# Kernel optimization log

Measured on AMD Instinct MI355X. Metric: run time of the kernel, lower is better.

## Reference

```python
import jax, jax.numpy as jnp
import numpy as np

B, S, QD, KVD, H = 8, 1024, 1024, 1024, 8
NEG_SLOPE = 0.01


def _lin(t, w, b):
    # torch nn.Linear: y = x @ W^T + b, W is (out, in)
    return t @ w.T + b


def _heads(t, n_head):
    b, s, e = t.shape
    return t.reshape(b, s, n_head, e // n_head).transpose(0, 2, 1, 3)  # (B,H,S,D)


def _merge(t):
    b, h, s, d = t.shape
    return t.transpose(0, 2, 1, 3).reshape(b, s, h * d)


def setup_inputs() -> dict:
    key = jax.random.key(0)
    ks = iter(jax.random.split(key, 64))

    def W(shape):
        return (jax.random.normal(next(ks), shape, jnp.float32) * 0.02)

    inp = {
        'x': jax.random.normal(next(ks), (B, S, QD), jnp.float32),
        'y': jax.random.normal(next(ks), (B, S, KVD), jnp.float32),
        # cross-attention projections
        'ca_q_w': W((QD, QD)), 'ca_q_b': W((QD,)),
        'ca_qv_w': W((QD, QD)), 'ca_qv_b': W((QD,)),
        'ca_k_w': W((QD, KVD)), 'ca_k_b': W((QD,)),
        'ca_kv_w': W((QD, KVD)), 'ca_kv_b': W((QD,)),
        'ca_o_w': W((QD, QD)), 'ca_o_b': W((QD,)),
        # LayerNorm over [seq_len, q_dim]
        'ln_w': jnp.ones((S, QD), jnp.float32),
        'ln_b': jnp.zeros((S, QD), jnp.float32),
        # 3-layer FeedForward
        'ff1_w': W((QD, QD)), 'ff1_b': W((QD,)),
        'ff2_w': W((QD, QD)), 'ff2_b': W((QD,)),
        'ff3_w': W((QD, QD)), 'ff3_b': W((QD,)),
        # self-attention 1
        'sa1_q_w': W((QD, QD)), 'sa1_q_b': W((QD,)),
        'sa1_k_w': W((QD, QD)), 'sa1_k_b': W((QD,)),
        'sa1_v_w': W((QD, QD)), 'sa1_v_b': W((QD,)),
        'sa1_o_w': W((QD, QD)), 'sa1_o_b': W((QD,)),
        # self-attention 2
        'sa2_q_w': W((QD, QD)), 'sa2_q_b': W((QD,)),
        'sa2_k_w': W((QD, QD)), 'sa2_k_b': W((QD,)),
        'sa2_v_w': W((QD, QD)), 'sa2_v_b': W((QD,)),
        'sa2_o_w': W((QD, QD)), 'sa2_o_b': W((QD,)),
    }
    return inp


def _self_attn(t, qw, qb, kw, kb, vw, vb, ow, ob):
    q = _heads(_lin(t, qw, qb), H)
    k = _heads(_lin(t, kw, kb), H)
    v = _heads(_lin(t, vw, vb), H)
    scale = 1.0 / jnp.sqrt(jnp.asarray(q.shape[-1], q.dtype))
    a = jax.nn.softmax(jnp.einsum('bhsd,bhtd->bhst', q, k) * scale, axis=-1)
    return _lin(_merge(jnp.einsum('bhst,bhtd->bhsd', a, v)), ow, ob)


def reference(x, y, ca_q_w, ca_q_b, ca_qv_w, ca_qv_b, ca_k_w, ca_k_b, ca_kv_w, ca_kv_b, ca_o_w, ca_o_b, ln_w, ln_b, ff1_w, ff1_b, ff2_w, ff2_b, ff3_w, ff3_b, sa1_q_w, sa1_q_b, sa1_k_w, sa1_k_b, sa1_v_w, sa1_v_b, sa1_o_w, sa1_o_b, sa2_q_w, sa2_q_b, sa2_k_w, sa2_k_b, sa2_v_w, sa2_v_b, sa2_o_w, sa2_o_b):
    # --- FlowFace cross-attention (no 1/sqrt(d) scaling, +QV term) ---
    q = _heads(_lin(x, ca_q_w, ca_q_b), H)
    qv = _heads(_lin(x, ca_qv_w, ca_qv_b), H)
    k = _heads(_lin(y, ca_k_w, ca_k_b), H)
    kv = _heads(_lin(y, ca_kv_w, ca_kv_b), H)
    attn = jax.nn.softmax(jnp.einsum('bhsd,bhtd->bhst', q, k), axis=-1)
    ca = _lin(_merge(jnp.einsum('bhst,bhtd->bhsd', attn, kv) + qv), ca_o_w, ca_o_b)
    h1 = x + ca
    # --- LayerNorm over last two dims [seq_len, q_dim] ---
    mu = h1.mean(axis=(-2, -1), keepdims=True)
    var = h1.var(axis=(-2, -1), keepdims=True)
    hn = (h1 - mu) / jnp.sqrt(var + 1e-5) * ln_w + ln_b
    # --- 3-layer FeedForward with leaky_relu + residual ---
    lr = lambda t: jax.nn.leaky_relu(t, NEG_SLOPE)
    f = lr(_lin(lr(_lin(lr(_lin(hn, ff1_w, ff1_b)), ff2_w, ff2_b)), ff3_w, ff3_b))
    h2 = hn + f
    # --- two self-attention layers ---
    h3 = _self_attn(h2, sa1_q_w, sa1_q_b, sa1_k_w, sa1_k_b, sa1_v_w, sa1_v_b, sa1_o_w, sa1_o_b)
    out = _self_attn(h3, sa2_q_w, sa2_q_b, sa2_k_w, sa2_k_b, sa2_v_w, sa2_v_b, sa2_o_w, sa2_o_b)
    return out
```

## Files before the change

### kernel.cpp

```cpp
#include <hip/hip_runtime.h>
#include <cstdint>
#include <cstddef>

#define DI __device__ __forceinline__

typedef __bf16 bf16x8 __attribute__((ext_vector_type(8)));
typedef float  f32x4  __attribute__((ext_vector_type(4)));

constexpr int kE = 1024;
constexpr int kM = 8192;
constexpr float kSlope = 0.01f;

DI float bf2f(ushort u) { union { uint32_t i; float f; } v; v.i = ((uint32_t)u) << 16; return v.f; }
DI ushort f2bf(float f) {
    union { float f; uint32_t i; } v; v.f = f;
    return (ushort)((v.i + 0x7FFFu + ((v.i >> 16) & 1u)) >> 16);
}
DI bf16x8 ld8f(const float* p) {
    const float4 f0 = *(const float4*)p;
    const float4 f1 = *(const float4*)(p + 4);
    union { bf16x8 v; ushort u[8]; } o;
    o.u[0] = f2bf(f0.x); o.u[1] = f2bf(f0.y); o.u[2] = f2bf(f0.z); o.u[3] = f2bf(f0.w);
    o.u[4] = f2bf(f1.x); o.u[5] = f2bf(f1.y); o.u[6] = f2bf(f1.z); o.u[7] = f2bf(f1.w);
    return o.v;
}
template<typename T> DI float ldf(const T* p);
template<> DI float ldf<ushort>(const ushort* p) { return bf2f(*p); }
template<> DI float ldf<float>(const float* p) { return *p; }

DI void gload16(const void* g, void* lds) {
    __builtin_amdgcn_global_load_lds((const __attribute__((address_space(1))) void*)g,
                                     (__attribute__((address_space(3))) void*)lds, 16, 0, 0);
}

DI int swz7(int r) { return ((r ^ (r >> 3)) & 7) << 4; }

struct PtrTab { const float* w[16]; const float* b[16]; const float* x; const float* y; };

__global__ __launch_bounds__(256)
void cvt_pack(PtrTab t, ushort* __restrict__ WB, ushort* __restrict__ Xb,
              ushort* __restrict__ Yb, float* __restrict__ BP)
{
    const int blk = blockIdx.x, tid = threadIdx.x;
    if (blk < 16384) {
        const float* src; ushort* dst; size_t idx;
        if (blk < 8192)       { const int w = blk >> 9; idx = (size_t)(blk & 511) * 2048 + tid * 8; src = t.w[w]; dst = WB + (size_t)w * 1048576; }
        else if (blk < 12288) { idx = (size_t)(blk - 8192) * 2048 + tid * 8;  src = t.x; dst = Xb; }
        else                  { idx = (size_t)(blk - 12288) * 2048 + tid * 8; src = t.y; dst = Yb; }
        *(bf16x8*)(dst + idx) = ld8f(src + idx);
    } else {
        const size_t i = (size_t)(blk - 16384) * 2048 + tid * 8;
        const int w = (int)(i >> 10), off = (int)(i & 1023);
        *(float4*)(BP + i)     = *(const float4*)(t.b[w] + off);
        *(float4*)(BP + i + 4) = *(const float4*)(t.b[w] + off + 4);
    }
}

template<int ACT, int RESID, int VT, typename TR, typename TO>
__global__ __launch_bounds__(256)
void gemm_bf16(const ushort* __restrict__ A, const ushort* __restrict__ W,
               const float* __restrict__ bias, const TR* __restrict__ resb,
               TO* __restrict__ out, int N, ushort* __restrict__ vt_out, int vtcol0,
               float oscale)
{
    __shared__ __align__(16) char sm[2][16384];
    constexpr int K = 1024;
    const int tid = threadIdx.x, l = tid & 63, wid = tid >> 6;
    const int wm = wid >> 1, wn = wid & 1;

    const int cpx = gridDim.x >> 3;
    const int sb = (blockIdx.x & 7) * cpx + (blockIdx.x >> 3);
    const int slab = sb >> 9, rr = sb & 511;
    const int bm = rr >> 3, bn = (slab << 3) + (rr & 7);
    const size_t row0 = (size_t)bm << 7, col0 = (size_t)bn << 7;
    const bool isvt = VT && ((int)col0 >= vtcol0);

    const int o0 = (wid * 2) * 1024 + (l << 4), o1 = o0 + 1024;
    const int r0s = o0 >> 6, c0s = ((o0 >> 4) & 3) ^ ((r0s >> 1) & 3);
    const int r1s = o1 >> 6, c1s = ((o1 >> 4) & 3) ^ ((r1s >> 1) & 3);
    const ushort* gA0 = A + (row0 + r0s) * K + c0s * 8;
    const ushort* gA1 = A + (row0 + r1s) * K + c1s * 8;
    const ushort* gW0 = W + (col0 + r0s) * K + c0s * 8;
    const ushort* gW1 = W + (col0 + r1s) * K + c1s * 8;
    const int d0 = (wid * 2) * 1024, d1 = d0 + 1024;

    f32x4 acc[4][4] = {};

    {
        gload16(gA0, sm[0] + d0); gload16(gA1, sm[0] + d1);
        gload16(gW0, sm[0] + 8192 + d0); gload16(gW1, sm[0] + 8192 + d1);
    }
    __syncthreads();

    for (int kt = 0; kt < 32; ++kt) {
        const int cur = kt & 1;
        if (kt + 1 < 32) {
            const int ko = (kt + 1) << 5;
            char* nb = sm[cur ^ 1];
            gload16(gA0 + ko, nb + d0); gload16(gA1 + ko, nb + d1);
            gload16(gW0 + ko, nb + 8192 + d0); gload16(gW1 + ko, nb + 8192 + d1);
        }
        const char* At = sm[cur];
        const char* Wt = sm[cur] + 8192;
        bf16x8 af[4], bfr[4];
        #pragma unroll
        for (int mi = 0; mi < 4; ++mi) {
            const int r = (wm << 6) + (mi << 4) + (l & 15);
            af[mi] = *(const bf16x8*)(At + r * 64 + ((((l >> 4) ^ ((r >> 1) & 3))) << 4));
        }
        #pragma unroll
        for (int ni = 0; ni < 4; ++ni) {
            const int r = (wn << 6) + (ni << 4) + (l & 15);
            bfr[ni] = *(const bf16x8*)(Wt + r * 64 + ((((l >> 4) ^ ((r >> 1) & 3))) << 4));
        }
        if (!isvt) {
            #pragma unroll
            for (int mi = 0; mi < 4; ++mi)
                #pragma unroll
                for (int ni = 0; ni < 4; ++ni)
                    acc[mi][ni] = __builtin_amdgcn_mfma_f32_16x16x32_bf16(af[mi], bfr[ni], acc[mi][ni], 0, 0, 0);
        } else {
            #pragma unroll
            for (int mi = 0; mi < 4; ++mi)
                #pragma unroll
                for (int ni = 0; ni < 4; ++ni)
                    acc[mi][ni] = __builtin_amdgcn_mfma_f32_16x16x32_bf16(bfr[ni], af[mi], acc[mi][ni], 0, 0, 0);
        }
        __syncthreads();
    }

    const int cr = (l >> 4) << 2, cc = l & 15;
    if (!isvt) {
        #pragma unroll
        for (int mi = 0; mi < 4; ++mi) {
            #pragma unroll
            for (int ni = 0; ni < 4; ++ni) {
                const size_t gr = row0 + (wm << 6) + (mi << 4) + cr;
                const size_t gc = col0 + (wn << 6) + (ni << 4) + cc;
                const float bv = bias[gc];
                #pragma unroll
                for (int r = 0; r < 4; ++r) {
                    float v = (acc[mi][ni][r] + bv) * oscale;
                    if (ACT) v = v > 0.f ? v : v * kSlope;
                    const size_t off = (gr + r) * (size_t)N + gc;
                    if (RESID) v += ldf(resb + off);
                    if constexpr (sizeof(TO) == 4) out[off] = v;
                    else                           out[off] = f2bf(v);
                }
            }
        }
    } else if (VT) {
        #pragma unroll
        for (int mi = 0; mi < 4; ++mi) {
            const size_t t_glob = row0 + (wm << 6) + (mi << 4) + cc;
            const size_t bb = t_glob >> 10;
            const int tt = (int)(t_glob & 1023);
            #pragma unroll
            for (int ni = 0; ni < 4; ++ni) {
                const int gcb = (int)col0 + (wn << 6) + (ni << 4) + cr;
                const int dbase = gcb - vtcol0;
                #pragma unroll
                for (int r = 0; r < 4; ++r) {
                    const float v = acc[mi][ni][r] + bias[gcb + r];
                    vt_out[(((bb << 10) + dbase + r) << 10) + tt] = f2bf(v);
                }
            }
        }
    }
}

template<int ADD_QV>
__global__ __launch_bounds__(256)
void attn_fwd(const ushort* __restrict__ Q, const ushort* __restrict__ K,
              const ushort* __restrict__ VT, const ushort* __restrict__ QV,
              ushort* __restrict__ O, int ld)
{
    __shared__ __align__(16) char Kt[64 * 256];
    __shared__ __align__(16) char Vt[128 * 128];
    __shared__ __align__(16) char Pl[4][2048];

    const int tid = threadIdx.x;
    const int l = tid & 63, w = tid >> 6;

    const int cpx = gridDim.x >> 3;
    const int sb = (blockIdx.x & 7) * cpx + (blockIdx.x >> 3);
    const int qt = sb & 15;
    const int bh = sb >> 4;
    const int h = bh & 7, b = bh >> 3;

    const size_t bi = ((size_t)b << 10) * (size_t)ld + ((size_t)h << 7);
    const size_t bo = ((size_t)b << 10) * 1024 + ((size_t)h << 7);
    const size_t vtoff = ((size_t)bh) << 17;
    const size_t qrow0 = (size_t)(qt << 6) + (w << 4);

    bf16x8 qf[4];
    #pragma unroll
    for (int kk = 0; kk < 4; ++kk)
        qf[kk] = *(const bf16x8*)(Q + bi + (qrow0 + (l & 15)) * ld + (kk << 5) + ((l >> 4) << 3));

    f32x4 oacc[8] = {};
    f32x4 lacc = {};
    float mrow[4] = {-1e30f, -1e30f, -1e30f, -1e30f};

    bf16x8 vones;
    #pragma unroll
    for (int j = 0; j < 8; ++j) vones[j] = (__bf16)1.0f;

    const int sr = tid >> 4, sc = tid & 15;

    int vofs[4];
    #pragma unroll
    for (int it = 0; it < 4; ++it) {
        const int d = it * 32 + (tid >> 3);
        const int s = tid & 7;
        const int c = s ^ ((d ^ (d >> 3)) & 7);
        vofs[it] = d * 1024 + c * 8;
    }
    const int vdst = tid * 16;

    for (int kt0 = 0; kt0 < 16; ++kt0) {
        __syncthreads();
        #pragma unroll
        for (int it = 0; it < 4; ++it) {
            const int r = sr + (it << 4);
            uint4 kv = *(const uint4*)(K + bi + (size_t)(kt0 * 64 + r) * ld + (sc << 3));
            *(uint4*)(Kt + r * 256 + ((sc << 4) ^ swz7(r))) = kv;
        }
        #pragma unroll
        for (int it = 0; it < 4; ++it) {
            uint4 vv = *(const uint4*)(VT + vtoff + (size_t)(kt0 << 6) + vofs[it]);
            *(uint4*)(Vt + it * 4096 + vdst) = vv;
        }
        __syncthreads();

        f32x4 sacc[4] = {};
        #pragma unroll
        for (int ni = 0; ni < 4; ++ni) {
            const int r = (l & 15) + (ni << 4);
            #pragma unroll
            for (int kk = 0; kk < 4; ++kk) {
                bf16x8 kf = *(const bf16x8*)(Kt + r * 256 + ((((kk << 2) + (l >> 4)) << 4) ^ swz7(r)));
                sacc[ni] = __builtin_amdgcn_mfma_f32_16x16x32_bf16(qf[kk], kf, sacc[ni], 0, 0, 0);
            }
        }

        float m0[4];
        #pragma unroll
        for (int r = 0; r < 4; ++r) {
            float m = fmaxf(fmaxf(sacc[0][r], sacc[1][r]), fmaxf(sacc[2][r], sacc[3][r]));
            #pragma unroll
            for (int msk = 1; msk < 16; msk <<= 1) m = fmaxf(m, __shfl_xor(m, msk, 64));
            m0[r] = m;
        }
        const bool grow = (m0[0] > mrow[0]) || (m0[1] > mrow[1]) ||
                          (m0[2] > mrow[2]) || (m0[3] > mrow[3]);
        if (__any(grow)) {
            float corr[4];
            #pragma unroll
            for (int r = 0; r < 4; ++r) {
                const float mn = fmaxf(mrow[r], m0[r]);
                corr[r] = __expf(mrow[r] - mn);
                mrow[r] = mn;
            }
            #pragma unroll
            for (int nd = 0; nd < 8; ++nd)
                #pragma unroll
                for (int r = 0; r < 4; ++r) oacc[nd][r] *= corr[r];
            #pragma unroll
            for (int r = 0; r < 4; ++r) lacc[r] *= corr[r];
        }

        char* pw = Pl[w];
        #pragma unroll
        for (int r = 0; r < 4; ++r) {
            const int q = ((l >> 4) << 2) + r;
            const int qo = q * 128, qm = swz7(q);
            const float mr = mrow[r];
            #pragma unroll
            for (int ni = 0; ni < 4; ++ni) {
                const float p = __expf(sacc[ni][r] - mr);
                const int t = (l & 15) + (ni << 4);
                *(__bf16*)(pw + qo + ((t * 2) ^ qm)) = (__bf16)p;
            }
        }

        #pragma unroll
        for (int tg = 0; tg < 2; ++tg) {
            const int q = l & 15;
            bf16x8 pf = *(const bf16x8*)(pw + q * 128 + ((((tg << 2) + (l >> 4)) << 4) ^ swz7(q)));
            #pragma unroll
            for (int nd = 0; nd < 8; ++nd) {
                const int d = (nd << 4) + (l & 15);
                const int m = (d ^ (d >> 3)) & 7;
                bf16x8 vf = *(const bf16x8*)(Vt + d * 128 + ((((tg << 2) + (l >> 4)) ^ m) << 4));
                oacc[nd] = __builtin_amdgcn_mfma_f32_16x16x32_bf16(pf, vf, oacc[nd], 0, 0, 0);
            }
            lacc = __builtin_amdgcn_mfma_f32_16x16x32_bf16(pf, vones, lacc, 0, 0, 0);
        }
    }

    const size_t orow = qrow0 + ((l >> 4) << 2);
    #pragma unroll
    for (int r = 0; r < 4; ++r) {
        const float inv = 1.f / lacc[r];
        #pragma unroll
        for (int nd = 0; nd < 8; ++nd) {
            const size_t c = (l & 15) + (nd << 4);
            float v = oacc[nd][r] * inv;
            if (ADD_QV) v += bf2f(QV[bi + (orow + r) * ld + c]);
            O[bo + (orow + r) * 1024 + c] = f2bf(v);
        }
    }
}

__global__ void ln_partial(const ushort* __restrict__ h1, float2* __restrict__ part)
{
    __shared__ float sa[8];
    const size_t off = ((size_t)blockIdx.x) << 15;
    float s = 0.f, s2 = 0.f;
    for (int i = threadIdx.x; i < 4096; i += 256) {
        uint4 u = *(const uint4*)(h1 + off + (size_t)i * 8);
        const ushort* e = (const ushort*)&u;
        #pragma unroll
        for (int j = 0; j < 8; ++j) { const float v = bf2f(e[j]); s += v; s2 += v * v; }
    }
    #pragma unroll
    for (int m = 1; m < 64; m <<= 1) { s += __shfl_xor(s, m, 64); s2 += __shfl_xor(s2, m, 64); }
    const int w = threadIdx.x >> 6;
    if ((threadIdx.x & 63) == 0) { sa[w * 2] = s; sa[w * 2 + 1] = s2; }
    __syncthreads();
    if (threadIdx.x == 0)
        part[blockIdx.x] = make_float2(sa[0] + sa[2] + sa[4] + sa[6], sa[1] + sa[3] + sa[5] + sa[7]);
}

__global__ void ln_finish(const float2* __restrict__ part, float2* __restrict__ stats)
{
    const int b = threadIdx.x;
    if (b < 8) {
        float s = 0.f, s2 = 0.f;
        for (int c = 0; c < 32; ++c) { const float2 v = part[b * 32 + c]; s += v.x; s2 += v.y; }
        const float mu = s * (1.f / 1048576.f);
        const float var = s2 * (1.f / 1048576.f) - mu * mu;
        stats[b] = make_float2(mu, rsqrtf(var + 1e-5f));
    }
}

__global__ void ln_apply(const ushort* __restrict__ h1, const float2* __restrict__ stats,
                         const float* __restrict__ gw, const float* __restrict__ gb,
                         ushort* __restrict__ hn)
{
    const size_t i = ((size_t)blockIdx.x * 256 + threadIdx.x) * 8;
    const int b = (int)(i >> 20);
    const size_t r = i & 1048575;
    const float2 st = stats[b];
    uint4 uv = *(const uint4*)(h1 + i);
    const float4 w0 = *(const float4*)(gw + r);
    const float4 w1 = *(const float4*)(gw + r + 4);
    const float4 b0 = *(const float4*)(gb + r);
    const float4 b1 = *(const float4*)(gb + r + 4);
    const float wv[8] = {w0.x, w0.y, w0.z, w0.w, w1.x, w1.y, w1.z, w1.w};
    const float bv[8] = {b0.x, b0.y, b0.z, b0.w, b1.x, b1.y, b1.z, b1.w};
    const ushort* ev = (const ushort*)&uv;
    ushort o[8];
    #pragma unroll
    for (int j = 0; j < 8; ++j)
        o[j] = f2bf((bf2f(ev[j]) - st.x) * st.y * wv[j] + bv[j]);
    *(uint4*)(hn + i) = *(const uint4*)o;
}

extern "C" void kernel_launch(void* const* d_in, const int* in_sizes, int n_in,
                              void* d_out, int out_size, void* d_ws, size_t ws_size,
                              hipStream_t stream)
{
    (void)in_sizes; (void)n_in; (void)out_size; (void)ws_size;
    auto P = [&](int i) { return (const float*)d_in[i]; };

    const size_t MB = 1u << 20;
    char* ws = (char*)d_ws;
    ushort* WB = (ushort*)ws;
    ushort* B0 = (ushort*)(ws + 32 * MB);
    ushort* B1 = (ushort*)(ws + 48 * MB);
    ushort* B2 = (ushort*)(ws + 64 * MB);
    ushort* B3 = (ushort*)(ws + 80 * MB);
    ushort* B4 = (ushort*)(ws + 96 * MB);
    ushort* B5 = (ushort*)(ws + 112 * MB);
    float*  BP = (float*)(ws + 128 * MB);
    float2* PART = (float2*)(ws + 128 * MB + 65536);
    float2* STATS = PART + 256;

    PtrTab tab;
    const int wsrc[16] = {2,4,6,8,10,14,16,18,20,22,24,26,28,30,32,34};
    for (int i = 0; i < 16; ++i) { tab.w[i] = P(wsrc[i]); tab.b[i] = P(wsrc[i] + 1); }
    tab.x = P(0); tab.y = P(1);

    const dim3 blk(256), gg(512);
    const float SA_SCALE = 0.08838834764831845f;
    auto Wp = [&](int w) { return WB + (size_t)w * 1048576; };
    auto Bp = [&](int w) { return BP + (size_t)w * 1024; };
    const ushort* NUS = nullptr;

    cvt_pack<<<dim3(16392), blk, 0, stream>>>(tab, WB, B4, B5, BP);

    gemm_bf16<0,0,0,ushort,ushort><<<gg, blk, 0, stream>>>(B4, Wp(0), Bp(0), NUS, B0, 1024, nullptr, 0, 1.0f);
    gemm_bf16<0,0,0,ushort,ushort><<<gg, blk, 0, stream>>>(B4, Wp(1), Bp(1), NUS, B1, 1024, nullptr, 0, 1.0f);
    gemm_bf16<0,0,0,ushort,ushort><<<gg, blk, 0, stream>>>(B5, Wp(2), Bp(2), NUS, B2, 1024, nullptr, 0, 1.0f);
    gemm_bf16<0,0,1,ushort,ushort><<<gg, blk, 0, stream>>>(B5, Wp(3), Bp(3), NUS, B3, 1024, B3, 0, 1.0f);
    attn_fwd<1><<<dim3(1024), blk, 0, stream>>>(B0, B2, B3, B1, B4, 1024);
    gemm_bf16<0,1,0,float,ushort><<<gg, blk, 0, stream>>>(B4, Wp(4), Bp(4), P(0), B5, 1024, nullptr, 0, 1.0f);

    ln_partial<<<dim3(256), blk, 0, stream>>>(B5, PART);
    ln_finish<<<dim3(1), dim3(64), 0, stream>>>(PART, STATS);
    ln_apply<<<dim3(4096), blk, 0, stream>>>(B5, STATS, P(12), P(13), B0);

    gemm_bf16<1,0,0,ushort,ushort><<<gg, blk, 0, stream>>>(B0, Wp(5), Bp(5), NUS, B1, 1024, nullptr, 0, 1.0f);
    gemm_bf16<1,0,0,ushort,ushort><<<gg, blk, 0, stream>>>(B1, Wp(6), Bp(6), NUS, B2, 1024, nullptr, 0, 1.0f);
    gemm_bf16<1,1,0,ushort,ushort><<<gg, blk, 0, stream>>>(B2, Wp(7), Bp(7), B0, B3, 1024, nullptr, 0, 1.0f);

    gemm_bf16<0,0,0,ushort,ushort><<<gg, blk, 0, stream>>>(B3, Wp(8),  Bp(8),  NUS, B0, 1024, nullptr, 0, SA_SCALE);
    gemm_bf16<0,0,0,ushort,ushort><<<gg, blk, 0, stream>>>(B3, Wp(9),  Bp(9),  NUS, B1, 1024, nullptr, 0, 1.0f);
    gemm_bf16<0,0,1,ushort,ushort><<<gg, blk, 0, stream>>>(B3, Wp(10), Bp(10), NUS, B2, 1024, B2, 0, 1.0f);
    attn_fwd<0><<<dim3(1024), blk, 0, stream>>>(B0, B1, B2, nullptr, B4, 1024);
    gemm_bf16<0,0,0,ushort,ushort><<<gg, blk, 0, stream>>>(B4, Wp(11), Bp(11), NUS, B5, 1024, nullptr, 0, 1.0f);

    gemm_bf16<0,0,0,ushort,ushort><<<gg, blk, 0, stream>>>(B5, Wp(12), Bp(12), NUS, B0, 1024, nullptr, 0, SA_SCALE);
    gemm_bf16<0,0,0,ushort,ushort><<<gg, blk, 0, stream>>>(B5, Wp(13), Bp(13), NUS, B1, 1024, nullptr, 0, 1.0f);
    gemm_bf16<0,0,1,ushort,ushort><<<gg, blk, 0, stream>>>(B5, Wp(14), Bp(14), NUS, B2, 1024, B2, 0, 1.0f);
    attn_fwd<0><<<dim3(1024), blk, 0, stream>>>(B0, B1, B2, nullptr, B4, 1024);
    gemm_bf16<0,0,0,ushort,float><<<gg, blk, 0, stream>>>(B4, Wp(15), Bp(15), NUS, (float*)d_out, 1024, nullptr, 0, 1.0f);
}
```

Baseline: 763.7 us.

## Double-buffer K/V tiles in attention with async global-to-LDS loads

```diff
diff --git a/kernel.cpp b/kernel.cpp
--- a/kernel.cpp
+++ b/kernel.cpp
@@ -175,8 +175,8 @@
               const ushort* __restrict__ VT, const ushort* __restrict__ QV,
               ushort* __restrict__ O, int ld)
 {
-    __shared__ __align__(16) char Kt[64 * 256];
-    __shared__ __align__(16) char Vt[128 * 128];
+    __shared__ __align__(16) char KB[2][16384];
+    __shared__ __align__(16) char VB[2][16384];
     __shared__ __align__(16) char Pl[4][2048];
 
     const int tid = threadIdx.x;
@@ -206,32 +206,44 @@
     #pragma unroll
     for (int j = 0; j < 8; ++j) vones[j] = (__bf16)1.0f;
 
-    const int sr = tid >> 4, sc = tid & 15;
-
-    int vofs[4];
-    #pragma unroll
-    for (int it = 0; it < 4; ++it) {
-        const int d = it * 32 + (tid >> 3);
-        const int s = tid & 7;
-        const int c = s ^ ((d ^ (d >> 3)) & 7);
-        vofs[it] = d * 1024 + c * 8;
-    }
-    const int vdst = tid * 16;
+    const int kr0 = (w << 4) + 0 + (l >> 4), kr1 = kr0 + 4, kr2 = kr0 + 8, kr3 = kr0 + 12;
+    const int ksl = l & 15;
+    const size_t ks0 = bi + (size_t)kr0 * ld + ((ksl ^ ((kr0 ^ (kr0 >> 3)) & 7)) << 3);
+    const size_t ks1 = bi + (size_t)kr1 * ld + ((ksl ^ ((kr1 ^ (kr1 >> 3)) & 7)) << 3);
+    const size_t ks2 = bi + (size_t)kr2 * ld + ((ksl ^ ((kr2 ^ (kr2 >> 3)) & 7)) << 3);
+    const size_t ks3 = bi + (size_t)kr3 * ld + ((ksl ^ ((kr3 ^ (kr3 >> 3)) & 7)) << 3);
+    const int vd0 = (w << 5) + 0 + (l >> 3), vd1 = vd0 + 8, vd2 = vd0 + 16, vd3 = vd0 + 24;
+    const int vsl = l & 7;
+    const size_t vs0 = vtoff + (size_t)vd0 * 1024 + ((vsl ^ ((vd0 ^ (vd0 >> 3)) & 7)) << 3);
+    const size_t vs1 = vtoff + (size_t)vd1 * 1024 + ((vsl ^ ((vd1 ^ (vd1 >> 3)) & 7)) << 3);
+    const size_t vs2 = vtoff + (size_t)vd2 * 1024 + ((vsl ^ ((vd2 ^ (vd2 >> 3)) & 7)) << 3);
+    const size_t vs3 = vtoff + (size_t)vd3 * 1024 + ((vsl ^ ((vd3 ^ (vd3 >> 3)) & 7)) << 3);
+    const int wb = w << 12;
+
+#define STAGE(KT, BUF)                                                         \
+    {                                                                          \
+        const size_t ko = (size_t)((KT) * 64) * (size_t)ld;                    \
+        char* kb = KB[BUF];                                                    \
+        gload16(K + ks0 + ko, kb + wb);                                        \
+        gload16(K + ks1 + ko, kb + wb + 1024);                                 \
+        gload16(K + ks2 + ko, kb + wb + 2048);                                 \
+        gload16(K + ks3 + ko, kb + wb + 3072);                                 \
+        const size_t vo = (size_t)((KT) << 6);                                 \
+        char* vb = VB[BUF];                                                    \
+        gload16(VT + vs0 + vo, vb + wb);                                       \
+        gload16(VT + vs1 + vo, vb + wb + 1024);                                \
+        gload16(VT + vs2 + vo, vb + wb + 2048);                                \
+        gload16(VT + vs3 + vo, vb + wb + 3072);                                \
+    }
+
+    STAGE(0, 0);
+    __syncthreads();
 
     for (int kt0 = 0; kt0 < 16; ++kt0) {
-        __syncthreads();
-        #pragma unroll
-        for (int it = 0; it < 4; ++it) {
-            const int r = sr + (it << 4);
-            uint4 kv = *(const uint4*)(K + bi + (size_t)(kt0 * 64 + r) * ld + (sc << 3));
-            *(uint4*)(Kt + r * 256 + ((sc << 4) ^ swz7(r))) = kv;
-        }
-        #pragma unroll
-        for (int it = 0; it < 4; ++it) {
-            uint4 vv = *(const uint4*)(VT + vtoff + (size_t)(kt0 << 6) + vofs[it]);
-            *(uint4*)(Vt + it * 4096 + vdst) = vv;
-        }
-        __syncthreads();
+        const int cur = kt0 & 1;
+        if (kt0 + 1 < 16) STAGE(kt0 + 1, cur ^ 1);
+        const char* Kt = KB[cur];
+        const char* Vt = VB[cur];
 
         f32x4 sacc[4] = {};
         #pragma unroll
@@ -297,7 +309,10 @@
             }
             lacc = __builtin_amdgcn_mfma_f32_16x16x32_bf16(pf, vones, lacc, 0, 0, 0);
         }
-    }
+
+        __syncthreads();
+    }
+#undef STAGE
 
     const size_t orow = qrow0 + ((l >> 4) << 2);
     #pragma unroll
```

Result: no change. 759.8 us (-0.5%).
